# Performance work log

Measured on AMD Instinct MI355X. Metric: run time of the kernel, lower is better.

The kernel has to match this reference:

```python
import jax, jax.numpy as jnp
import numpy as np

N_NODES = 50000
DIM = 256
N_EDGES = 320000


def setup_inputs() -> dict:
    key = jax.random.key(0)
    k1, k2, k3, k4 = jax.random.split(key, 4)
    nodes = jnp.arange(N_NODES, dtype=jnp.int64) if jax.config.jax_enable_x64 else jnp.arange(N_NODES, dtype=jnp.int32)
    edges = jax.random.randint(k1, (2, N_EDGES), 0, N_NODES)
    emb_table = jax.random.normal(k2, (N_NODES, DIM), dtype=jnp.float32)
    W = jax.random.normal(k3, (DIM, DIM), dtype=jnp.float32) * (1.0 / np.sqrt(DIM))
    b = jax.random.normal(k4, (DIM,), dtype=jnp.float32) * 0.01
    return {"nodes": nodes, "edges": edges, "emb_table": emb_table, "W": W, "b": b}


def reference(nodes, edges, emb_table, W, b):
    # Embedding lookup
    x = emb_table[nodes]                       # [N, D]
    n = x.shape[0]
    # GCNConv: linear transform first (torch Linear: x @ W^T)
    x = x @ W.T                                # [N, D]
    # Add self-loops
    loop = jnp.arange(n, dtype=edges.dtype)
    src = jnp.concatenate([edges[0], loop])    # [E+N]
    dst = jnp.concatenate([edges[1], loop])
    # Symmetric normalization: deg over destination nodes
    deg = jax.ops.segment_sum(jnp.ones_like(src, dtype=x.dtype), dst, num_segments=n)
    dinv = jnp.where(deg > 0, jax.lax.rsqrt(jnp.maximum(deg, 1e-12)), 0.0)
    norm = dinv[src] * dinv[dst]               # [E+N]
    # Gather-scale-scatter aggregation
    msg = x[src] * norm[:, None]               # [E+N, D]
    out = jax.ops.segment_sum(msg, dst, num_segments=n)
    out = out + b
    return jax.nn.relu(out)
```

## Files before the change

kernel.cpp:

```cpp
#include <hip/hip_runtime.h>
#include <hip/hip_bf16.h>

#define N_NODES 50000
#define DIM 256
#define N_EDGES 320000
#define BM 32
#define LDA 264
#define SCAN_NB 196

typedef __attribute__((ext_vector_type(8))) short short8;
typedef __attribute__((ext_vector_type(4))) float f32x4;
typedef __attribute__((ext_vector_type(4))) unsigned short ushort4v;

struct alignas(8) Pay { int idx; float nrm; };

static __device__ __forceinline__ unsigned short f2bf(float f) {
  unsigned int u = __float_as_uint(f);
  return (unsigned short)((u + 0x7FFFu + ((u >> 16) & 1u)) >> 16);
}
static __device__ __forceinline__ float bf2f(unsigned short s) {
  return __uint_as_float(((unsigned int)s) << 16);
}

template <int FULL>
__global__ __launch_bounds__(256) void k_misc(const float* __restrict__ emb,
                                              unsigned short* __restrict__ ebf,
                                              const float* __restrict__ W,
                                              unsigned short* __restrict__ wbf,
                                              const int* __restrict__ dst,
                                              int* __restrict__ deg) {
  const int EB = FULL ? 12500 : 0;
  int b = blockIdx.x;
  if (FULL && b < EB) {
    int i = b * 256 + threadIdx.x;
    const float4 v = ((const float4*)emb)[i];
    ushort4v r;
    r.x = f2bf(v.x); r.y = f2bf(v.y); r.z = f2bf(v.z); r.w = f2bf(v.w);
    *(ushort4v*)(ebf + (size_t)i * 4) = r;
  } else if (b < EB + 64) {
    int i = (b - EB) * 256 + threadIdx.x;
    const float4 v = ((const float4*)W)[i];
    ushort4v r;
    r.x = f2bf(v.x); r.y = f2bf(v.y); r.z = f2bf(v.z); r.w = f2bf(v.w);
    *(ushort4v*)(wbf + (size_t)i * 4) = r;
  } else {
    int e = (b - EB - 64) * 256 + threadIdx.x;
    if (e < N_EDGES) atomicAdd(&deg[dst[e]], 1);
  }
}

__global__ __launch_bounds__(256) void k_scan1(const int* __restrict__ deg,
                                               int* __restrict__ bsum) {
  int i = blockIdx.x * 256 + threadIdx.x;
  int v = (i < N_NODES) ? deg[i] : 0;
#pragma unroll
  for (int off = 32; off; off >>= 1) v += __shfl_xor(v, off, 64);
  __shared__ int ws[4];
  if ((threadIdx.x & 63) == 0) ws[threadIdx.x >> 6] = v;
  __syncthreads();
  if (threadIdx.x == 0) bsum[blockIdx.x] = ws[0] + ws[1] + ws[2] + ws[3];
}

__global__ __launch_bounds__(256) void k_scan2(const int* __restrict__ bsum,
                                               int* __restrict__ bbase) {
  __shared__ int wsum[4], wb[4];
  int tid = threadIdx.x, lane = tid & 63, wv = tid >> 6;
  int v = (tid < SCAN_NB) ? bsum[tid] : 0;
  int x = v;
#pragma unroll
  for (int off = 1; off < 64; off <<= 1) {
    int y = __shfl_up(x, off, 64);
    if (lane >= off) x += y;
  }
  if (lane == 63) wsum[wv] = x;
  __syncthreads();
  if (tid == 0) { int s = 0; for (int k = 0; k < 4; ++k) { int t = wsum[k]; wb[k] = s; s += t; } }
  __syncthreads();
  if (tid < SCAN_NB) bbase[tid] = wb[wv] + (x - v);
}

__global__ __launch_bounds__(256) void k_scan3(const int* __restrict__ deg,
                                               const int* __restrict__ bbase,
                                               int* __restrict__ offs,
                                               int* __restrict__ cursor,
                                               float* __restrict__ dinv) {
  __shared__ int wsum[4], wb[4];
  int tid = threadIdx.x, lane = tid & 63, wv = tid >> 6;
  int i = blockIdx.x * 256 + tid;
  int v = (i < N_NODES) ? deg[i] : 0;
  int x = v;
#pragma unroll
  for (int off = 1; off < 64; off <<= 1) {
    int y = __shfl_up(x, off, 64);
    if (lane >= off) x += y;
  }
  if (lane == 63) wsum[wv] = x;
  __syncthreads();
  if (tid == 0) { int s = 0; for (int k = 0; k < 4; ++k) { int t = wsum[k]; wb[k] = s; s += t; } }
  __syncthreads();
  if (i < N_NODES) {
    int excl = bbase[blockIdx.x] + wb[wv] + (x - v);
    offs[i] = excl;
    cursor[i] = excl;
    dinv[i] = rsqrtf((float)(v + 1));
  }
  if (blockIdx.x == 0 && tid == 0) offs[N_NODES] = N_EDGES;
}

__global__ __launch_bounds__(256) void k_scatter(const int* __restrict__ src,
                                                 const int* __restrict__ dst,
                                                 const int* __restrict__ nodes,
                                                 const float* __restrict__ dinv,
                                                 int* __restrict__ cursor,
                                                 Pay* __restrict__ pay) {
  int e = blockIdx.x * 256 + threadIdx.x;
  if (e >= N_EDGES) return;
  int s = src[e], d = dst[e];
  int pos = atomicAdd(&cursor[d], 1);
  Pay p;
  p.idx = nodes[s];
  p.nrm = dinv[s] * dinv[d];
  pay[pos] = p;
}

template <int EMBBF>
__global__ __launch_bounds__(256) void k_gather(const int* __restrict__ nodes,
                                                const float* __restrict__ dinv,
                                                const void* __restrict__ embv,
                                                const int* __restrict__ offs,
                                                const Pay* __restrict__ pay,
                                                unsigned short* __restrict__ agg) {
  int d = (blockIdx.x * 256 + threadIdx.x) >> 6;
  if (d >= N_NODES) return;
  const int lane = threadIdx.x & 63;
  const float dd = dinv[d];
  const int nr = nodes[d];
  const float sl = dd * dd;
  float4 acc;
  if (EMBBF) {
    const ushort4v s4 = ((const ushort4v*)((const unsigned short*)embv + (size_t)nr * DIM))[lane];
    acc = make_float4(bf2f(s4.x) * sl, bf2f(s4.y) * sl, bf2f(s4.z) * sl, bf2f(s4.w) * sl);
  } else {
    const float4 v = ((const float4*)((const float*)embv + (size_t)nr * DIM))[lane];
    acc = make_float4(v.x * sl, v.y * sl, v.z * sl, v.w * sl);
  }
  const int jb = offs[d], je = offs[d + 1];
  int e = jb;
  for (; e + 4 <= je; e += 4) {
    const Pay p0 = pay[e], p1 = pay[e + 1], p2 = pay[e + 2], p3 = pay[e + 3];
    if (EMBBF) {
      const unsigned short* eb = (const unsigned short*)embv;
      const ushort4v w0 = ((const ushort4v*)(eb + (size_t)p0.idx * DIM))[lane];
      const ushort4v w1 = ((const ushort4v*)(eb + (size_t)p1.idx * DIM))[lane];
      const ushort4v w2 = ((const ushort4v*)(eb + (size_t)p2.idx * DIM))[lane];
      const ushort4v w3 = ((const ushort4v*)(eb + (size_t)p3.idx * DIM))[lane];
      acc.x += bf2f(w0.x) * p0.nrm + bf2f(w1.x) * p1.nrm + bf2f(w2.x) * p2.nrm + bf2f(w3.x) * p3.nrm;
      acc.y += bf2f(w0.y) * p0.nrm + bf2f(w1.y) * p1.nrm + bf2f(w2.y) * p2.nrm + bf2f(w3.y) * p3.nrm;
      acc.z += bf2f(w0.z) * p0.nrm + bf2f(w1.z) * p1.nrm + bf2f(w2.z) * p2.nrm + bf2f(w3.z) * p3.nrm;
      acc.w += bf2f(w0.w) * p0.nrm + bf2f(w1.w) * p1.nrm + bf2f(w2.w) * p2.nrm + bf2f(w3.w) * p3.nrm;
    } else {
      const float* ef = (const float*)embv;
      const float4 w0 = ((const float4*)(ef + (size_t)p0.idx * DIM))[lane];
      const float4 w1 = ((const float4*)(ef + (size_t)p1.idx * DIM))[lane];
      const float4 w2 = ((const float4*)(ef + (size_t)p2.idx * DIM))[lane];
      const float4 w3 = ((const float4*)(ef + (size_t)p3.idx * DIM))[lane];
      acc.x += w0.x * p0.nrm + w1.x * p1.nrm + w2.x * p2.nrm + w3.x * p3.nrm;
      acc.y += w0.y * p0.nrm + w1.y * p1.nrm + w2.y * p2.nrm + w3.y * p3.nrm;
      acc.z += w0.z * p0.nrm + w1.z * p1.nrm + w2.z * p2.nrm + w3.z * p3.nrm;
      acc.w += w0.w * p0.nrm + w1.w * p1.nrm + w2.w * p2.nrm + w3.w * p3.nrm;
    }
  }
  for (; e < je; ++e) {
    const Pay p = pay[e];
    if (EMBBF) {
      const ushort4v w = ((const ushort4v*)((const unsigned short*)embv + (size_t)p.idx * DIM))[lane];
      acc.x += bf2f(w.x) * p.nrm; acc.y += bf2f(w.y) * p.nrm;
      acc.z += bf2f(w.z) * p.nrm; acc.w += bf2f(w.w) * p.nrm;
    } else {
      const float4 w = ((const float4*)((const float*)embv + (size_t)p.idx * DIM))[lane];
      acc.x += w.x * p.nrm; acc.y += w.y * p.nrm;
      acc.z += w.z * p.nrm; acc.w += w.w * p.nrm;
    }
  }
  ushort4v o;
  o.x = f2bf(acc.x); o.y = f2bf(acc.y); o.z = f2bf(acc.z); o.w = f2bf(acc.w);
  ((ushort4v*)(agg + (size_t)d * DIM))[lane] = o;
}

__global__ __launch_bounds__(256) void k_gemm(const unsigned short* __restrict__ agg,
                                              const unsigned short* __restrict__ wbf,
                                              const float* __restrict__ bias,
                                              float* __restrict__ out) {
  __shared__ unsigned short As[BM * LDA];
  const int tid = threadIdx.x;
  const int row0 = blockIdx.x * BM;

  {
    const int c = (tid & 31) * 8;
    const int rb = tid >> 5;
#pragma unroll
    for (int p = 0; p < 4; ++p) {
      const int r = rb + p * 8;
      const int grow = row0 + r;
      short8 v = {};
      if (grow < N_NODES) v = *(const short8*)(agg + (size_t)grow * DIM + c);
      *(short8*)&As[r * LDA + c] = v;
    }
  }
  __syncthreads();

  const int wv = tid >> 6, lane = tid & 63;
  const int l15 = lane & 15, kq = lane >> 4;
  const int cb = wv * 64;
  f32x4 acc[2][4] = {};
#pragma unroll
  for (int ks = 0; ks < 8; ++ks) {
    const int kb = ks * 32 + kq * 8;
    short8 a0 = *(const short8*)&As[l15 * LDA + kb];
    short8 a1 = *(const short8*)&As[(16 + l15) * LDA + kb];
    short8 b[4];
#pragma unroll
    for (int f = 0; f < 4; ++f)
      b[f] = *(const short8*)(wbf + (cb + f * 16 + l15) * 256 + kb);
#pragma unroll
    for (int f = 0; f < 4; ++f) {
      acc[0][f] = __builtin_amdgcn_mfma_f32_16x16x32_bf16(a0, b[f], acc[0][f], 0, 0, 0);
      acc[1][f] = __builtin_amdgcn_mfma_f32_16x16x32_bf16(a1, b[f], acc[1][f], 0, 0, 0);
    }
  }
#pragma unroll
  for (int h = 0; h < 2; ++h) {
    int rb = row0 + h * 16 + kq * 4;
#pragma unroll
    for (int f = 0; f < 4; ++f) {
      int col = cb + f * 16 + l15;
      float bv = bias[col];
#pragma unroll
      for (int g = 0; g < 4; ++g) {
        int r = rb + g;
        if (r < N_NODES) {
          float v = acc[h][f][g] + bv;
          __builtin_nontemporal_store(fmaxf(v, 0.f), &out[(size_t)r * DIM + col]);
        }
      }
    }
  }
}

extern "C" void kernel_launch(void* const* d_in, const int* in_sizes, int n_in,
                              void* d_out, int out_size, void* d_ws, size_t ws_size,
                              hipStream_t stream) {
  const int* nodes = (const int*)d_in[0];
  const int* edges = (const int*)d_in[1];
  const float* emb = (const float*)d_in[2];
  const float* W = (const float*)d_in[3];
  const float* bias = (const float*)d_in[4];
  float* out = (float*)d_out;

  int* deg = (int*)d_ws;
  float* dinv = (float*)((char*)d_ws + 200704);
  int* offs = (int*)((char*)d_ws + 401408);
  int* cursor = (int*)((char*)d_ws + 602112);
  int* bsum = (int*)((char*)d_ws + 802816);
  int* bbase = (int*)((char*)d_ws + 803840);
  unsigned short* wbf = (unsigned short*)((char*)d_ws + 804864);
  Pay* pay = (Pay*)((char*)d_ws + 935936);
  unsigned short* ebf = (unsigned short*)((char*)d_ws + 3495936);
  unsigned short* agg = (unsigned short*)((char*)d_ws + 29095936);
  const bool full = ws_size >= 54695936ull;
  if (!full) agg = (unsigned short*)((char*)d_ws + 3495936);

  const int* srcp = edges;
  const int* dstp = edges + N_EDGES;

  hipMemsetAsync(deg, 0, N_NODES * sizeof(int), stream);
  if (full)
    k_misc<1><<<12500 + 64 + 1250, 256, 0, stream>>>(emb, ebf, W, wbf, dstp, deg);
  else
    k_misc<0><<<64 + 1250, 256, 0, stream>>>(emb, ebf, W, wbf, dstp, deg);
  k_scan1<<<SCAN_NB, 256, 0, stream>>>(deg, bsum);
  k_scan2<<<1, 256, 0, stream>>>(bsum, bbase);
  k_scan3<<<SCAN_NB, 256, 0, stream>>>(deg, bbase, offs, cursor, dinv);
  k_scatter<<<(N_EDGES + 255) / 256, 256, 0, stream>>>(srcp, dstp, nodes, dinv, cursor, pay);
  if (full)
    k_gather<1><<<(N_NODES * 64 + 255) / 256, 256, 0, stream>>>(nodes, dinv, ebf, offs, pay, agg);
  else
    k_gather<0><<<(N_NODES * 64 + 255) / 256, 256, 0, stream>>>(nodes, dinv, emb, offs, pay, agg);
  k_gemm<<<(N_NODES + BM - 1) / BM, 256, 0, stream>>>(agg, wbf, bias, out);
}
```

Baseline: 216.5 us.

## Make GEMM persistent with register-resident W and double-buffered A prefetch

The GEMM kernel becomes a persistent grid of 521 blocks, each looping over row tiles. Each block loads its W fragments and bias into registers once. The next tile's aggregated rows are prefetched into registers while the current tile computes, using a double-buffered LDS tile. This removes repeated W reads per tile and hides agg load latency. The cost is much higher register pressure (32 short8 W fragments per thread), which may reduce occupancy or cause spills.

```diff
diff --git a/kernel.cpp b/kernel.cpp
--- a/kernel.cpp
+++ b/kernel.cpp
@@ -7,6 +7,8 @@
 #define BM 32
 #define LDA 264
 #define SCAN_NB 196
+#define GEMM_NT ((N_NODES + BM - 1) / BM)
+#define GEMM_GRID 521
 
 typedef __attribute__((ext_vector_type(8))) short short8;
 typedef __attribute__((ext_vector_type(4))) float f32x4;
@@ -191,59 +193,84 @@
                                               const unsigned short* __restrict__ wbf,
                                               const float* __restrict__ bias,
                                               float* __restrict__ out) {
-  __shared__ unsigned short As[BM * LDA];
+  __shared__ unsigned short As[2][BM * LDA];
   const int tid = threadIdx.x;
-  const int row0 = blockIdx.x * BM;
-
-  {
-    const int c = (tid & 31) * 8;
-    const int rb = tid >> 5;
-#pragma unroll
-    for (int p = 0; p < 4; ++p) {
-      const int r = rb + p * 8;
-      const int grow = row0 + r;
-      short8 v = {};
-      if (grow < N_NODES) v = *(const short8*)(agg + (size_t)grow * DIM + c);
-      *(short8*)&As[r * LDA + c] = v;
-    }
-  }
-  __syncthreads();
-
   const int wv = tid >> 6, lane = tid & 63;
   const int l15 = lane & 15, kq = lane >> 4;
   const int cb = wv * 64;
-  f32x4 acc[2][4] = {};
-#pragma unroll
-  for (int ks = 0; ks < 8; ++ks) {
-    const int kb = ks * 32 + kq * 8;
-    short8 a0 = *(const short8*)&As[l15 * LDA + kb];
-    short8 a1 = *(const short8*)&As[(16 + l15) * LDA + kb];
-    short8 b[4];
+
+  short8 bf[8][4];
+#pragma unroll
+  for (int ks = 0; ks < 8; ++ks)
 #pragma unroll
     for (int f = 0; f < 4; ++f)
-      b[f] = *(const short8*)(wbf + (cb + f * 16 + l15) * 256 + kb);
-#pragma unroll
-    for (int f = 0; f < 4; ++f) {
-      acc[0][f] = __builtin_amdgcn_mfma_f32_16x16x32_bf16(a0, b[f], acc[0][f], 0, 0, 0);
-      acc[1][f] = __builtin_amdgcn_mfma_f32_16x16x32_bf16(a1, b[f], acc[1][f], 0, 0, 0);
-    }
-  }
-#pragma unroll
-  for (int h = 0; h < 2; ++h) {
-    int rb = row0 + h * 16 + kq * 4;
-#pragma unroll
-    for (int f = 0; f < 4; ++f) {
-      int col = cb + f * 16 + l15;
-      float bv = bias[col];
-#pragma unroll
-      for (int g = 0; g < 4; ++g) {
-        int r = rb + g;
-        if (r < N_NODES) {
-          float v = acc[h][f][g] + bv;
-          __builtin_nontemporal_store(fmaxf(v, 0.f), &out[(size_t)r * DIM + col]);
+      bf[ks][f] = *(const short8*)(wbf + (size_t)(cb + f * 16 + l15) * 256 + ks * 32 + kq * 8);
+  float bv[4];
+#pragma unroll
+  for (int f = 0; f < 4; ++f) bv[f] = bias[cb + f * 16 + l15];
+
+  const int c = (tid & 31) * 8;
+  const int rb = tid >> 5;
+
+  int t = blockIdx.x;
+  short8 pre[4];
+#pragma unroll
+  for (int p = 0; p < 4; ++p) {
+    const int grow = t * BM + rb + p * 8;
+    short8 v = {};
+    if (grow < N_NODES) v = *(const short8*)(agg + (size_t)grow * DIM + c);
+    pre[p] = v;
+  }
+
+  int cur = 0;
+  for (; t < GEMM_NT; t += gridDim.x) {
+#pragma unroll
+    for (int p = 0; p < 4; ++p)
+      *(short8*)&As[cur][(rb + p * 8) * LDA + c] = pre[p];
+    __syncthreads();
+
+    const int tn = t + gridDim.x;
+    if (tn < GEMM_NT) {
+#pragma unroll
+      for (int p = 0; p < 4; ++p) {
+        const int grow = tn * BM + rb + p * 8;
+        short8 v = {};
+        if (grow < N_NODES) v = *(const short8*)(agg + (size_t)grow * DIM + c);
+        pre[p] = v;
+      }
+    }
+
+    f32x4 acc[2][4] = {};
+#pragma unroll
+    for (int ks = 0; ks < 8; ++ks) {
+      const int kb = ks * 32 + kq * 8;
+      short8 a0 = *(const short8*)&As[cur][l15 * LDA + kb];
+      short8 a1 = *(const short8*)&As[cur][(16 + l15) * LDA + kb];
+#pragma unroll
+      for (int f = 0; f < 4; ++f) {
+        acc[0][f] = __builtin_amdgcn_mfma_f32_16x16x32_bf16(a0, bf[ks][f], acc[0][f], 0, 0, 0);
+        acc[1][f] = __builtin_amdgcn_mfma_f32_16x16x32_bf16(a1, bf[ks][f], acc[1][f], 0, 0, 0);
+      }
+    }
+
+    const int row0 = t * BM;
+#pragma unroll
+    for (int h = 0; h < 2; ++h) {
+      int rbo = row0 + h * 16 + kq * 4;
+#pragma unroll
+      for (int f = 0; f < 4; ++f) {
+        int col = cb + f * 16 + l15;
+#pragma unroll
+        for (int g = 0; g < 4; ++g) {
+          int r = rbo + g;
+          if (r < N_NODES) {
+            float v = acc[h][f][g] + bv[f];
+            __builtin_nontemporal_store(fmaxf(v, 0.f), &out[(size_t)r * DIM + col]);
+          }
         }
       }
     }
+    cur ^= 1;
   }
 }
 
@@ -286,5 +313,5 @@
     k_gather<1><<<(N_NODES * 64 + 255) / 256, 256, 0, stream>>>(nodes, dinv, ebf, offs, pay, agg);
   else
     k_gather<0><<<(N_NODES * 64 + 255) / 256, 256, 0, stream>>>(nodes, dinv, emb, offs, pay, agg);
-  k_gemm<<<(N_NODES + BM - 1) / BM, 256, 0, stream>>>(agg, wbf, bias, out);
-}
+  k_gemm<<<GEMM_GRID, 256, 0, stream>>>(agg, wbf, bias, out);
+}
```

After: 200.7 us. -7.3%, faster.
